# Kernel optimization log

Measured on AMD Instinct MI355X. Metric: run time of the kernel, lower is better.

## Reference

```python
import jax, jax.numpy as jnp
import numpy as np

B, T_IN, T_OUT, N, D_IN, D_OUT, H, L, K = 32, 12, 12, 200, 2, 1, 128, 2, 2
DH = H // 2
M = 2 * K + 1  # identity + K diffusion steps for each of the 2 supports
SQRT_H = float(np.sqrt(H))


def setup_inputs():
    key = jax.random.key(0)
    ks = iter(jax.random.split(key, 40))
    def rn(shape, s=0.1):
        return jax.random.normal(next(ks), shape, dtype=jnp.float32) * s
    return {
        "encoder_inputs": rn((B, T_IN, N, D_IN), 1.0),
        "decoder_inputs": rn((B, T_OUT, N, D_OUT), 1.0),
        "gru_Wih": rn((3 * H, D_IN)), "gru_Whh": rn((3 * H, H)),
        "gru_bih": rn((3 * H,)), "gru_bhh": rn((3 * H,)),
        "att_W": rn((DH, H)), "att_b": rn((DH,)),
        "w_len_C": rn((DH, 1)), "w_key": rn((H, DH)), "w_query": rn((H, DH)),
        "enc_Wg0": rn(((D_IN + H) * M, 2 * H)), "enc_bg0": rn((2 * H,)),
        "enc_Wc0": rn(((D_IN + H) * M, H)), "enc_bc0": rn((H,)),
        "enc_Wg1": rn((2 * H * M, 2 * H)), "enc_bg1": rn((2 * H,)),
        "enc_Wc1": rn((2 * H * M, H)), "enc_bc1": rn((H,)),
        "dec_Wg0": rn(((D_OUT + H) * M, 2 * H)), "dec_bg0": rn((2 * H,)),
        "dec_Wc0": rn(((D_OUT + H) * M, H)), "dec_bc0": rn((H,)),
        "dec_Wg1": rn((2 * H * M, 2 * H)), "dec_bg1": rn((2 * H,)),
        "dec_Wc1": rn((2 * H * M, H)), "dec_bc1": rn((H,)),
        "proj_W": rn((D_OUT, H)), "proj_b": rn((D_OUT,)),
        "top_k": 20,
    }


def _gconv(supports, x, W, b):
    # x: (B, N, D); supports: list of (B, N, N). Chebyshev-style diffusion.
    xs = [x]
    for s in supports:
        x0, x1 = x, jnp.einsum('bij,bjd->bid', s, x)
        xs.append(x1)
        for _ in range(2, K + 1):
            x2 = 2.0 * jnp.einsum('bij,bjd->bid', s, x1) - x0
            xs.append(x2)
            x0, x1 = x1, x2
    xm = jnp.stack(xs, axis=-1).reshape(x.shape[0], x.shape[1], -1)  # (B,N,D*M)
    return xm @ W + b


def _cell(supports, inp, h, Wg, bg, Wc, bc):
    # DCGRU cell: diffusion-conv GRU gating. inp (B,N,di), h (B,N,H)
    ru = jax.nn.sigmoid(_gconv(supports, jnp.concatenate([inp, h], -1), Wg, bg))
    r, u = ru[..., :H], ru[..., H:]
    c = jnp.tanh(_gconv(supports, jnp.concatenate([inp, r * h], -1), Wc, bc))
    return u * h + (1.0 - u) * c


def _supports(x, gru_Wih, gru_Whh, gru_bih, gru_bhh, att_W, att_b, w_len_C, w_key, w_query, top_k):
    # x: (B, T, N, D) -> per-node GRU over time (fold nodes into batch)
    xt = jnp.transpose(x, (1, 2, 0, 3)).reshape(T_IN, N * B, D_IN)
    def gru_step(h, xin):
        gi = xin @ gru_Wih.T + gru_bih
        gh = h @ gru_Whh.T + gru_bhh
        ir, iz, ig = jnp.split(gi, 3, -1)
        hr, hz, hg = jnp.split(gh, 3, -1)
        r = jax.nn.sigmoid(ir + hr)
        z = jax.nn.sigmoid(iz + hz)
        n = jnp.tanh(ig + r * hg)
        hnew = (1.0 - z) * n + z * h
        return hnew, hnew
    _, outs = jax.lax.scan(gru_step, jnp.zeros((N * B, H), x.dtype), xt)
    outs = outs.reshape(T_IN, N, B, H)
    # temporal attention pooling per node
    sc = jax.nn.relu(jnp.einsum('tnbh,dh->tnbd', outs, att_W) + att_b)
    att_t = jax.nn.softmax(jnp.einsum('tnbd,do->tnbo', sc, w_len_C)[..., 0], axis=0)  # (T,N,B)
    pooled = jnp.einsum('tnbh,tnb->bnh', outs, att_t)  # (B,N,H)
    # node-node attention -> sparsified adjacency
    keym = pooled @ w_key
    qm = pooled @ w_query
    attn = jax.nn.softmax(jnp.einsum('bnd,bmd->bnm', keym, qm) / SQRT_H, axis=-1)
    kth = jax.lax.top_k(attn, top_k)[0][..., -1:]  # k-th largest per row
    adj = jnp.where(attn >= kth, attn, 0.0) + jnp.eye(N, dtype=attn.dtype)
    def rw(a):  # D^-1 A, row-normalized random walk
        d = a.sum(-1)
        dinv = jnp.where(d == 0.0, 0.0, 1.0 / d)
        return dinv[..., None] * a
    s1 = jnp.transpose(rw(adj), (0, 2, 1))
    s2 = jnp.transpose(rw(jnp.transpose(adj, (0, 2, 1))), (0, 2, 1))
    return [s1, s2]


def _forward(encoder_inputs, decoder_inputs, gru_Wih, gru_Whh, gru_bih, gru_bhh,
             att_W, att_b, w_len_C, w_key, w_query,
             enc_Wg0, enc_bg0, enc_Wc0, enc_bc0, enc_Wg1, enc_bg1, enc_Wc1, enc_bc1,
             dec_Wg0, dec_bg0, dec_Wc0, dec_bc0, dec_Wg1, dec_bg1, dec_Wc1, dec_bc1,
             proj_W, proj_b, top_k):
    supports = _supports(encoder_inputs, gru_Wih, gru_Whh, gru_bih, gru_bhh,
                         att_W, att_b, w_len_C, w_key, w_query, top_k)
    enc = jnp.transpose(encoder_inputs, (1, 0, 2, 3))  # (T,B,N,Din)
    enc_params = [(enc_Wg0, enc_bg0, enc_Wc0, enc_bc0), (enc_Wg1, enc_bg1, enc_Wc1, enc_bc1)]
    dec_params = [(dec_Wg0, dec_bg0, dec_Wc0, dec_bc0), (dec_Wg1, dec_bg1, dec_Wc1, dec_bc1)]
    # encoder: scan over time per layer
    cur = enc
    hiddens = []
    for l in range(L):
        Wg, bg, Wc, bc = enc_params[l]
        def estep(h, xin, Wg=Wg, bg=bg, Wc=Wc, bc=bc):
            hn = _cell(supports, xin, h, Wg, bg, Wc, bc)
            return hn, hn
        hl, cur = jax.lax.scan(estep, jnp.zeros((B, N, H), enc.dtype), cur)
        hiddens.append(hl)
    go = jnp.zeros((B, N, D_OUT), enc.dtype)
    def dstep(carry, _):
        hs, x = carry
        hs_new = []
        for l in range(L):
            hn = _cell(supports, x, hs[l], *dec_params[l])
            x = hn
            hs_new.append(hn)
        proj = x @ proj_W.T + proj_b  # (B,N,D_OUT)
        return (tuple(hs_new), proj), proj.reshape(B, N * D_OUT)
    _, outputs = jax.lax.scan(dstep, (tuple(hiddens), go), None, length=T_OUT)
    return outputs  # (T_OUT, B, N*D_OUT)


def reference(encoder_inputs, decoder_inputs, gru_Wih, gru_Whh, gru_bih, gru_bhh,
              att_W, att_b, w_len_C, w_key, w_query,
              enc_Wg0, enc_bg0, enc_Wc0, enc_bc0, enc_Wg1, enc_bg1, enc_Wc1, enc_bc1,
              dec_Wg0, dec_bg0, dec_Wc0, dec_bc0, dec_Wg1, dec_bg1, dec_Wc1, dec_bc1,
              proj_W, proj_b, top_k):
    return _forward(encoder_inputs, decoder_inputs, gru_Wih, gru_Whh, gru_bih, gru_bhh,
                    att_W, att_b, w_len_C, w_key, w_query,
                    enc_Wg0, enc_bg0, enc_Wc0, enc_bc0, enc_Wg1, enc_bg1, enc_Wc1, enc_bc1,
                    dec_Wg0, dec_bg0, dec_Wc0, dec_bc0, dec_Wg1, dec_bg1, dec_Wc1, dec_bc1,
                    proj_W, proj_b, top_k)
```

## Files before the change

### kernel.cpp

```cpp
#include <hip/hip_runtime.h>
#include <hip/hip_bf16.h>
#include <math.h>

#define BB 32
#define T_INC 12
#define T_OUTC 12
#define NN 200
#define DIN0 2
#define HH 128
#define DHALF 64
#define NB (NN*BB)
#define XROW 256
#define MSTRIDE ((size_t)NB*XROW)
#define CHUNK 32
#define QT 2
#define KT2 7
#define RT2 13
#define SFRAG_PER_B ((size_t)RT2*KT2*64*8)
#define PANEL_E (KT2*QT*64*8)
#define GCONV_LDS (4*PANEL_E*2)
#define INV_SQRT_H 0.08838834764831845f

typedef __attribute__((ext_vector_type(8))) short bf16x8;
typedef __attribute__((ext_vector_type(4))) float f32x4;

__device__ __forceinline__ float sigmf(float x){ return 1.f/(1.f+expf(-x)); }
__device__ __forceinline__ float bfu(uint32_t b){ union{uint32_t u;float f;}v; v.u=b<<16; return v.f; }
__device__ __forceinline__ uint32_t fbf(float f){ union{float f2;uint32_t u;}v; v.f2=f; return (v.u + 0x7fffu + ((v.u>>16)&1u))>>16; }
__device__ __forceinline__ void splitbf(float v, uint32_t& hi, uint32_t& lo){
  hi = fbf(v);
  lo = fbf(v - bfu(hi));
}

__global__ void k_whhT(const float* __restrict__ Whh, float* __restrict__ WT) {
  int idx = blockIdx.x*256 + threadIdx.x;
  if (idx >= 3*HH*HH) return;
  int i3 = idx / HH; int k = idx % HH;
  WT[(size_t)k*(3*HH) + i3] = Whh[idx];
}

__global__ void k_wshuf(const float* __restrict__ W, __hip_bfloat16* __restrict__ Wfh,
                        __hip_bfloat16* __restrict__ Wfl, int d, int d_pad, int OUT) {
  int idx = blockIdx.x*256 + threadIdx.x;
  int total = 5*d_pad*OUT;
  if (idx >= total) return;
  int o = idx % OUT; int tmp = idx / OUT; int k = tmp % d_pad; int m = tmp / d_pad;
  float v = (k < d) ? W[((size_t)k*5 + m)*OUT + o] : 0.f;
  int kt = k >> 5, kr = k & 31;
  int lane = ((kr>>3)<<4) | (o & 15);
  int j = kr & 7;
  int nt = o >> 4;
  int KT = d_pad >> 5, NT = OUT >> 4;
  size_t addr = ((((size_t)m*KT + kt)*NT + nt)*64 + (size_t)lane)*8 + j;
  uint32_t hi, lo; splitbf(v, hi, lo);
  Wfh[addr] = *(__hip_bfloat16*)&hi;
  Wfl[addr] = *(__hip_bfloat16*)&lo;
}

__global__ void k_sshuf(const float* __restrict__ adj, const float* __restrict__ rs,
                        const float* __restrict__ cs,
                        __hip_bfloat16* __restrict__ SFH, __hip_bfloat16* __restrict__ SFL) {
  const int PER_B = 208*224;
  int idx = blockIdx.x*256 + threadIdx.x;
  if (idx >= 2*BB*PER_B) return;
  int e = idx % PER_B; int t2 = idx / PER_B; int b = t2 % BB; int mat = t2 / BB;
  int n = e / 224; int j = e % 224;
  float v = 0.f;
  if (n < NN && j < NN) {
    if (mat == 0) v = adj[((size_t)b*NN + j)*NN + n] / rs[(size_t)b*NN + j];
    else          v = adj[((size_t)b*NN + n)*NN + j] / cs[(size_t)b*NN + j];
  }
  int rt = n >> 4, rr = n & 15, kt = j >> 5, kr = j & 31;
  int lane = ((kr >> 3) << 4) | rr;
  int jj = kr & 7;
  size_t addr = ((size_t)(mat*BB + b)*RT2*KT2 + (size_t)(rt*KT2 + kt))*512
              + (size_t)lane*8 + jj;
  uint32_t hi, lo; splitbf(v, hi, lo);
  SFH[addr] = *(__hip_bfloat16*)&hi;
  SFL[addr] = *(__hip_bfloat16*)&lo;
}

__global__ __launch_bounds__(512) void k_gru_all(
    const float* __restrict__ enc_in, const float* __restrict__ Wih,
    const float* __restrict__ WhhT, const float* __restrict__ bih,
    const float* __restrict__ bhh, float* __restrict__ outs) {
  int row0 = blockIdx.x * 4;
  int tid = threadIdx.x;
  int rr = tid >> 7;
  int i = tid & 127;
  int row = row0 + rr;
  int n = row / BB, b = row % BB;
  __shared__ float hs[4][HH];
  hs[rr][i] = 0.f;
  float wi0 = Wih[(0*HH+i)*2+0], wi1 = Wih[(0*HH+i)*2+1];
  float wz0 = Wih[(1*HH+i)*2+0], wz1 = Wih[(1*HH+i)*2+1];
  float wg0 = Wih[(2*HH+i)*2+0], wg1 = Wih[(2*HH+i)*2+1];
  float bi = bih[i], bz = bih[HH+i], bg = bih[2*HH+i];
  float bhr = bhh[i], bhz = bhh[HH+i], bhg = bhh[2*HH+i];
  for (int t=0;t<T_INC;t++) {
    __syncthreads();
    float x0 = enc_in[(((size_t)b*T_INC + t)*NN + n)*DIN0 + 0];
    float x1 = enc_in[(((size_t)b*T_INC + t)*NN + n)*DIN0 + 1];
    float ir = wi0*x0 + wi1*x1 + bi;
    float iz = wz0*x0 + wz1*x1 + bz;
    float ig = wg0*x0 + wg1*x1 + bg;
    float hr = bhr, hz = bhz, hg = bhg;
    for (int k=0;k<HH;k++) {
      float hv = hs[rr][k];
      const float* wr = WhhT + (size_t)k*(3*HH);
      hr += wr[i]*hv; hz += wr[i+128]*hv; hg += wr[i+256]*hv;
    }
    float r = sigmf(ir+hr);
    float z = sigmf(iz+hz);
    float nn2 = tanhf(ig + r*hg);
    float hn = (1.f-z)*nn2 + z*hs[rr][i];
    __syncthreads();
    hs[rr][i] = hn;
    outs[(((size_t)t*NN+n)*BB+b)*HH + i] = hn;
  }
}

__global__ __launch_bounds__(256) void k_att_pool(
    const float* __restrict__ outs, const float* __restrict__ attW,
    const float* __restrict__ attb, const float* __restrict__ wlc,
    float* __restrict__ pooled) {
  int row = blockIdx.x; int n = row / BB, b = row % BB;
  int tid = threadIdx.x;
  __shared__ float o_s[T_INC][HH];
  __shared__ float aw[DHALF][HH+1];
  __shared__ float pt[T_INC];
  for (int i = tid; i < T_INC*HH; i += 256) {
    int t = i >> 7, k = i & 127;
    o_s[t][k] = outs[(((size_t)t*NN+n)*BB+b)*HH + k];
  }
  for (int i = tid; i < DHALF*HH; i += 256) {
    int d2 = i >> 7, k = i & 127;
    aw[d2][k] = attW[(size_t)d2*HH + k];
  }
  __syncthreads();
  int d = tid & 63, tq = tid >> 6;
  float ab = attb[d], wc = wlc[d];
  float part[3];
  #pragma unroll
  for (int j=0;j<3;j++) {
    int t = tq + j*4;
    float acc = ab;
    for (int k=0;k<HH;k++) acc += aw[d][k]*o_s[t][k];
    part[j] = fmaxf(acc, 0.f)*wc;
  }
  for (int off=32; off; off>>=1)
    #pragma unroll
    for (int j=0;j<3;j++) part[j] += __shfl_xor(part[j], off, 64);
  if (d == 0) { pt[tq] = part[0]; pt[tq+4] = part[1]; pt[tq+8] = part[2]; }
  __syncthreads();
  float mx = -1e30f;
  for (int t=0;t<T_INC;t++) mx = fmaxf(mx, pt[t]);
  float e[T_INC]; float s = 0.f;
  for (int t=0;t<T_INC;t++) { e[t] = expf(pt[t]-mx); s += e[t]; }
  float inv = 1.f/s;
  for (int k=tid;k<HH;k+=256) {
    float acc = 0.f;
    for (int t=0;t<T_INC;t++) acc += o_s[t][k]*e[t];
    pooled[((size_t)b*NN+n)*HH + k] = acc*inv;
  }
}

__global__ void k_keyquery(const float* __restrict__ pooled, const float* __restrict__ wkey,
                           const float* __restrict__ wqry, float* __restrict__ keym,
                           float* __restrict__ qm) {
  int bn = blockIdx.x; int lane = threadIdx.x;
  __shared__ float p_s[HH];
  p_s[lane] = pooled[(size_t)bn*HH + lane];
  p_s[lane+64] = pooled[(size_t)bn*HH + lane + 64];
  __syncthreads();
  float ka = 0.f, qa = 0.f;
  for (int k=0;k<HH;k++) {
    float pv = p_s[k];
    ka += pv*wkey[(size_t)k*DHALF + lane];
    qa += pv*wqry[(size_t)k*DHALF + lane];
  }
  keym[(size_t)bn*DHALF + lane] = ka;
  qm[(size_t)bn*DHALF + lane] = qa;
}

__global__ void k_attn_row(const float* __restrict__ keym, const float* __restrict__ qm,
                           const int* __restrict__ topkp, float* __restrict__ adj,
                           float* __restrict__ rowsum) {
  int bn = blockIdx.x; int b = bn / NN; int n = bn % NN;
  int tid = threadIdx.x;
  __shared__ float key_s[DHALF];
  __shared__ float attv[256];
  __shared__ float red[256];
  __shared__ int redi[256];
  if (tid < DHALF) key_s[tid] = keym[(size_t)bn*DHALF + tid];
  __syncthreads();
  float sc = -1e30f;
  if (tid < NN) {
    float a = 0.f;
    const float* qrow = qm + ((size_t)b*NN + tid)*DHALF;
    for (int k=0;k<DHALF;k++) a += key_s[k]*qrow[k];
    sc = a * INV_SQRT_H;
  }
  red[tid] = sc; __syncthreads();
  for (int s=128;s>0;s>>=1){ if (tid<s) red[tid]=fmaxf(red[tid],red[tid+s]); __syncthreads(); }
  float mx = red[0]; __syncthreads();
  float e = (tid<NN) ? expf(sc-mx) : 0.f;
  red[tid] = e; __syncthreads();
  for (int s=128;s>0;s>>=1){ if (tid<s) red[tid]+=red[tid+s]; __syncthreads(); }
  float inv = 1.f/red[0]; __syncthreads();
  float av = e*inv;
  attv[tid] = (tid<NN) ? av : -1e30f;
  __syncthreads();
  int Ks = topkp[0]; if (Ks > NN) Ks = NN;
  float kth = -1e30f;
  for (int it=0; it<Ks; it++) {
    red[tid] = attv[tid]; redi[tid] = tid; __syncthreads();
    for (int s=128;s>0;s>>=1){
      if (tid<s && red[tid+s] > red[tid]) { red[tid]=red[tid+s]; redi[tid]=redi[tid+s]; }
      __syncthreads();
    }
    kth = red[0];
    if (tid==0) attv[redi[0]] = -1e30f;
    __syncthreads();
  }
  float aout = 0.f;
  if (tid < NN) {
    aout = (av >= kth) ? av : 0.f;
    if (tid == n) aout += 1.f;
    adj[((size_t)b*NN+n)*NN + tid] = aout;
  }
  red[tid] = aout; __syncthreads();
  for (int s=128;s>0;s>>=1){ if (tid<s) red[tid]+=red[tid+s]; __syncthreads(); }
  if (tid==0) rowsum[bn] = red[0];
}

__global__ void k_colsum(const float* __restrict__ adj, float* __restrict__ cs) {
  int b = blockIdx.x;
  for (int j=threadIdx.x; j<NN; j+=blockDim.x) {
    float s = 0.f;
    for (int i=0;i<NN;i++) s += adj[((size_t)b*NN+i)*NN + j];
    cs[(size_t)b*NN + j] = s;
  }
}

__global__ __launch_bounds__(512) void k_gconv_mfma(
    const float* __restrict__ x, int bs, int ns, int din,
    const float* __restrict__ h, const float* __restrict__ ru,
    const __hip_bfloat16* __restrict__ SFH, const __hip_bfloat16* __restrict__ SFL,
    uint32_t* __restrict__ XP, int d) {
  extern __shared__ char ldsc[];
  ushort* X0H = (ushort*)ldsc;
  ushort* X0L = X0H + PANEL_E;
  ushort* XTH = X0L + PANEL_E;
  ushort* XTL = XTH + PANEL_E;
  int c0 = blockIdx.x*CHUNK;
  int b  = blockIdx.y;
  int tid = threadIdx.x;
  int l = tid & 63, wid = tid >> 6;

  { uint4 z = make_uint4(0,0,0,0);
    uint4* p = (uint4*)ldsc;
    for (int i = tid; i < GCONV_LDS/16; i += 512) p[i] = z; }
  __syncthreads();

  for (int i = tid; i < NN*CHUNK; i += 512) {
    int n = i >> 5, cc = i & 31;
    int c = c0 + cc;
    float v = 0.f;
    if (c < din) {
      v = x[(size_t)b*bs + (size_t)n*ns + c];
    } else if (c < d) {
      int k = c - din;
      v = h[((size_t)(b*NN+n))*HH + k];
      if (ru) v *= ru[(size_t)(b*NN+n)*256 + k];
    }
    uint32_t hi, lo; splitbf(v, hi, lo);
    int kt = n >> 5, kr = n & 31;
    int ln = ((kr>>3)<<4) | (cc & 15), jj = kr & 7, q = cc >> 4;
    int fa = ((kt*QT + q)*64 + ln)*8 + jj;
    X0H[fa] = (ushort)hi; X0L[fa] = (ushort)lo;
    XP[(size_t)(b*NN+n)*XROW + c] = hi | (lo << 16);
  }
  __syncthreads();

  for (int ph = 0; ph < 4; ph++) {
    int side = ph >> 1, cheb = ph & 1;
    const ushort* BH = cheb ? XTH : X0H;
    const ushort* BL = cheb ? XTL : X0L;
    const __hip_bfloat16* AH = SFH + (size_t)(side*BB + b)*SFRAG_PER_B;
    const __hip_bfloat16* AL = SFL + (size_t)(side*BB + b)*SFRAG_PER_B;
    int mout = 1 + ph;
    for (int rt = wid; rt < RT2; rt += 8) {
      f32x4 acc[QT];
      #pragma unroll
      for (int q=0;q<QT;q++) acc[q] = (f32x4){0.f,0.f,0.f,0.f};
      for (int kt = 0; kt < KT2; kt++) {
        size_t aoff = ((size_t)(rt*KT2+kt)*64 + l)*8;
        bf16x8 ah = *(const bf16x8*)(AH + aoff);
        bf16x8 al = *(const bf16x8*)(AL + aoff);
        #pragma unroll
        for (int q=0;q<QT;q++) {
          int boff = ((kt*QT+q)*64 + l)*8;
          bf16x8 bh = *(const bf16x8*)(BH + boff);
          bf16x8 bl = *(const bf16x8*)(BL + boff);
          acc[q] = __builtin_amdgcn_mfma_f32_16x16x32_bf16(ah, bl, acc[q], 0, 0, 0);
          acc[q] = __builtin_amdgcn_mfma_f32_16x16x32_bf16(al, bh, acc[q], 0, 0, 0);
          acc[q] = __builtin_amdgcn_mfma_f32_16x16x32_bf16(ah, bh, acc[q], 0, 0, 0);
        }
      }
      int colb = l & 15;
      #pragma unroll
      for (int q=0;q<QT;q++) {
        int cc = q*16 + colb;
        #pragma unroll
        for (int r=0;r<4;r++) {
          int n = rt*16 + ((l>>4)<<2) + r;
          float v = acc[q][r];
          int kt2 = n >> 5, kr = n & 31;
          int ln = ((kr>>3)<<4) | colb, jj = kr & 7;
          int fa = ((kt2*QT + q)*64 + ln)*8 + jj;
          if (cheb) {
            uint32_t h2 = X0H[fa], l2 = X0L[fa];
            v = 2.f*v - (bfu(h2) + bfu(l2));
          }
          uint32_t hi, lo; splitbf(v, hi, lo);
          if (!cheb) { XTH[fa] = (ushort)hi; XTL[fa] = (ushort)lo; }
          if (n < NN)
            XP[(size_t)mout*MSTRIDE + (size_t)(b*NN+n)*XROW + c0 + cc] = hi | (lo << 16);
        }
      }
    }
    __syncthreads();
  }
}

template<int OUT, int PATH>
__global__ __launch_bounds__(256) void k_dense_mfma(
    const uint32_t* __restrict__ XP,
    const __hip_bfloat16* __restrict__ Wfh, const __hip_bfloat16* __restrict__ Wfl,
    const float* __restrict__ bias, int d_pad,
    float* __restrict__ RU, const float* __restrict__ h, float* __restrict__ hnew,
    const float* __restrict__ pW, const float* __restrict__ pb,
    float* __restrict__ out, float* __restrict__ decx, int t) {
  __shared__ ushort SA[2*32*256];
  ushort* SAh = SA;
  ushort* SAl = SA + 32*256;
  int tid = threadIdx.x;
  int w = tid >> 6, l = tid & 63;
  int rblk = blockIdx.x*32;
  int rbase = (w&1)*16;
  int cbase = blockIdx.y*128 + (w>>1)*64;
  const int NT = OUT >> 4;
  int KT = d_pad >> 5;
  f32x4 acc[4];
  #pragma unroll
  for (int q=0;q<4;q++) acc[q] = (f32x4){0.f,0.f,0.f,0.f};
  size_t boff = (((size_t)(cbase>>4))*64 + l)*8;
  int ngrp = d_pad >> 3;
  for (int m=0;m<5;m++) {
    __syncthreads();
    for (int i = tid; i < 32*ngrp; i += 256) {
      int r = i / ngrp, cg = i % ngrp;
      const uint32_t* gp = XP + (size_t)m*MSTRIDE + (size_t)(rblk+r)*XROW + cg*8;
      uint4 p0 = *(const uint4*)gp;
      uint4 p1 = *(const uint4*)(gp+4);
      uint4 hv, lv;
      hv.x = (p0.x & 0xffffu) | (p0.y << 16);
      hv.y = (p0.z & 0xffffu) | (p0.w << 16);
      hv.z = (p1.x & 0xffffu) | (p1.y << 16);
      hv.w = (p1.z & 0xffffu) | (p1.w << 16);
      lv.x = (p0.x >> 16) | (p0.y & 0xffff0000u);
      lv.y = (p0.z >> 16) | (p0.w & 0xffff0000u);
      lv.z = (p1.x >> 16) | (p1.y & 0xffff0000u);
      lv.w = (p1.z >> 16) | (p1.w & 0xffff0000u);
      uint32_t bo2 = ((uint32_t)(r*256 + cg*8)*2) ^ ((uint32_t)(r&7)<<4);
      *(uint4*)((char*)SAh + bo2) = hv;
      *(uint4*)((char*)SAl + bo2) = lv;
    }
    __syncthreads();
    for (int kt=0; kt<KT; kt++) {
      int rr = rbase + (l & 15);
      uint32_t fb = ((uint32_t)(rr*256 + kt*32 + (l>>4)*8)*2) ^ ((uint32_t)(rr&7)<<4);
      bf16x8 ah = *(const bf16x8*)((const char*)SAh + fb);
      bf16x8 al = *(const bf16x8*)((const char*)SAl + fb);
      size_t bo = boff + ((size_t)(m*KT + kt)*NT)*512;
      #pragma unroll
      for (int q=0;q<4;q++) {
        bf16x8 bh = *(const bf16x8*)(Wfh + bo + (size_t)q*512);
        bf16x8 bl = *(const bf16x8*)(Wfl + bo + (size_t)q*512);
        acc[q] = __builtin_amdgcn_mfma_f32_16x16x32_bf16(ah, bl, acc[q], 0, 0, 0);
        acc[q] = __builtin_amdgcn_mfma_f32_16x16x32_bf16(al, bh, acc[q], 0, 0, 0);
        acc[q] = __builtin_amdgcn_mfma_f32_16x16x32_bf16(ah, bh, acc[q], 0, 0, 0);
      }
    }
  }
  bool doproj = (PATH==1) && (pW != nullptr);
  if (doproj) __syncthreads();
  float* PH = (float*)SA;
  int drow0 = rbase + ((l>>4)<<2);
  int col0 = l & 15;
  #pragma unroll
  for (int q=0;q<4;q++) {
    int col = cbase + q*16 + col0;
    float bv = bias[col];
    #pragma unroll
    for (int r=0;r<4;r++) {
      int rowrel = drow0 + r;
      int row = rblk + rowrel;
      float v = acc[q][r] + bv;
      if (PATH==0) {
        RU[(size_t)row*256 + col] = sigmf(v);
      } else {
        float c = tanhf(v);
        float u = RU[(size_t)row*256 + 128 + col];
        float hv = u*h[(size_t)row*HH + col] + (1.f-u)*c;
        hnew[(size_t)row*HH + col] = hv;
        if (doproj) PH[rowrel*HH + col] = hv;
      }
    }
  }
  if (doproj) {
    __syncthreads();
    int rowrel = tid >> 3;
    int sub = tid & 7;
    float s = 0.f;
    const float* ph = PH + rowrel*HH + sub*16;
    #pragma unroll
    for (int c=0;c<16;c++) s += ph[c]*pW[sub*16 + c];
    s += __shfl_xor(s, 1, 64);
    s += __shfl_xor(s, 2, 64);
    s += __shfl_xor(s, 4, 64);
    if (sub == 0) {
      float pv = s + pb[0];
      int gr = rblk + rowrel;
      out[(size_t)t*NB + gr] = pv;
      decx[gr] = pv;
    }
  }
}

extern "C" void kernel_launch(void* const* d_in, const int* in_sizes, int n_in,
                              void* d_out, int out_size, void* d_ws, size_t ws_size,
                              hipStream_t stream) {
  const float* enc_in = (const float*)d_in[0];
  const float* gWih = (const float*)d_in[2];
  const float* gWhh = (const float*)d_in[3];
  const float* gbih = (const float*)d_in[4];
  const float* gbhh = (const float*)d_in[5];
  const float* attW = (const float*)d_in[6];
  const float* attb = (const float*)d_in[7];
  const float* wlc  = (const float*)d_in[8];
  const float* wkey = (const float*)d_in[9];
  const float* wqry = (const float*)d_in[10];
  const float* cWg[4] = {(const float*)d_in[11],(const float*)d_in[15],(const float*)d_in[19],(const float*)d_in[23]};
  const float* cbg[4] = {(const float*)d_in[12],(const float*)d_in[16],(const float*)d_in[20],(const float*)d_in[24]};
  const float* cWc[4] = {(const float*)d_in[13],(const float*)d_in[17],(const float*)d_in[21],(const float*)d_in[25]};
  const float* cbc[4] = {(const float*)d_in[14],(const float*)d_in[18],(const float*)d_in[22],(const float*)d_in[26]};
  const float* pW = (const float*)d_in[27];
  const float* pb = (const float*)d_in[28];
  const int* topkp = (const int*)d_in[29];
  float* out = (float*)d_out;

  const int d_full[4] = {130, 256, 129, 256};
  const int d_padv[4] = {192, 256, 192, 256};

  float* ws = (float*)d_ws;
  size_t off = 0;
  auto alloc = [&](size_t n) { float* p = ws + off; off += (n + 255) & ~(size_t)255; return p; };

  float* RS   = alloc(NB);
  float* CS   = alloc(NB);
  float* RU   = alloc((size_t)NB*256);
  float* H0A  = alloc((size_t)NB*HH);
  float* H0B  = alloc((size_t)NB*HH);
  float* H1A  = alloc((size_t)NB*HH);
  float* H1B  = alloc((size_t)NB*HH);
  float* DECX = alloc(NB);
  float* WHHT = alloc((size_t)3*HH*HH);
  __hip_bfloat16* SFH = (__hip_bfloat16*)alloc((size_t)2*BB*SFRAG_PER_B/2);
  __hip_bfloat16* SFL = (__hip_bfloat16*)alloc((size_t)2*BB*SFRAG_PER_B/2);
  __hip_bfloat16 *WGFh[4], *WGFl[4], *WCFh[4], *WCFl[4];
  for (int p=0;p<4;p++) {
    WGFh[p] = (__hip_bfloat16*)alloc((size_t)5*d_padv[p]*256/2);
    WGFl[p] = (__hip_bfloat16*)alloc((size_t)5*d_padv[p]*256/2);
    WCFh[p] = (__hip_bfloat16*)alloc((size_t)5*d_padv[p]*128/2);
    WCFl[p] = (__hip_bfloat16*)alloc((size_t)5*d_padv[p]*128/2);
  }

  const size_t SUP_SZ = (size_t)T_INC*NN*BB*HH
                      + (size_t)NB*HH
                      + (size_t)NB*DHALF*2
                      + (size_t)BB*NN*NN + 4096;
  const size_t CELL_SZ = 5*MSTRIDE + 4096;
  float* UNION = alloc(SUP_SZ > CELL_SZ ? SUP_SZ : CELL_SZ);
  float* OUTS = UNION;
  float* POOL = OUTS + (size_t)T_INC*NN*BB*HH;
  float* KEYM = POOL + (size_t)NB*HH;
  float* QMM  = KEYM + (size_t)NB*DHALF;
  float* ADJ  = QMM  + (size_t)NB*DHALF;
  uint32_t* XP = (uint32_t*)UNION;

  if (off*sizeof(float) > ws_size) return;

  hipMemsetAsync(H0A, 0, (size_t)NB*HH*sizeof(float), stream);
  hipMemsetAsync(H1A, 0, (size_t)NB*HH*sizeof(float), stream);
  hipMemsetAsync(DECX, 0, (size_t)NB*sizeof(float), stream);

  k_whhT<<<(3*HH*HH+255)/256, 256, 0, stream>>>(gWhh, WHHT);
  for (int p=0;p<4;p++) {
    int tg = 5*d_padv[p]*256;
    k_wshuf<<<(tg+255)/256, 256, 0, stream>>>(cWg[p], WGFh[p], WGFl[p], d_full[p], d_padv[p], 256);
    int tc = 5*d_padv[p]*128;
    k_wshuf<<<(tc+255)/256, 256, 0, stream>>>(cWc[p], WCFh[p], WCFl[p], d_full[p], d_padv[p], 128);
  }

  k_gru_all<<<NB/4, 512, 0, stream>>>(enc_in, gWih, WHHT, gbih, gbhh, OUTS);
  k_att_pool<<<NB, 256, 0, stream>>>(OUTS, attW, attb, wlc, POOL);
  k_keyquery<<<NB, 64, 0, stream>>>(POOL, wkey, wqry, KEYM, QMM);
  k_attn_row<<<NB, 256, 0, stream>>>(KEYM, QMM, topkp, ADJ, RS);
  k_colsum<<<BB, 256, 0, stream>>>(ADJ, CS);
  { int tot = 2*BB*208*224;
    k_sshuf<<<(tot+255)/256, 256, 0, stream>>>(ADJ, RS, CS, SFH, SFL); }

  auto gconv = [&](const float* x, int bs, int ns, int din, const float* hcur,
                   const float* ru, int pidx) {
    int d = d_full[pidx], dp = d_padv[pidx];
    dim3 gg(dp/CHUNK, BB);
    k_gconv_mfma<<<gg, 512, GCONV_LDS, stream>>>(
        x, bs, ns, din, hcur, ru, SFH, SFL, XP, d);
  };

  auto cell = [&](const float* x, int bs, int ns, int din,
                  float** hcur, float** halt, int pidx, int t) {
    int dp = d_padv[pidx];
    gconv(x, bs, ns, din, *hcur, nullptr, pidx);
    k_dense_mfma<256,0><<<dim3(NB/32,2),256,0,stream>>>(
        XP, WGFh[pidx], WGFl[pidx], cbg[pidx], dp, RU, nullptr, nullptr,
        nullptr, nullptr, nullptr, nullptr, 0);
    gconv(x, bs, ns, din, *hcur, RU, pidx);
    const float* ppW = (pidx == 3) ? pW : nullptr;
    k_dense_mfma<128,1><<<dim3(NB/32,1),256,0,stream>>>(
        XP, WCFh[pidx], WCFl[pidx], cbc[pidx], dp, RU, *hcur, *halt,
        ppW, pb, out, DECX, t);
    float* tswp = *hcur; *hcur = *halt; *halt = tswp;
  };

  float* h0cur = H0A; float* h0alt = H0B;
  float* h1cur = H1A; float* h1alt = H1B;

  for (int t=0;t<T_INC;t++) {
    cell(enc_in + (size_t)t*NN*DIN0, T_INC*NN*DIN0, DIN0, DIN0, &h0cur, &h0alt, 0, 0);
    cell(h0cur, NN*HH, HH, HH, &h1cur, &h1alt, 1, 0);
  }
  for (int t=0;t<T_OUTC;t++) {
    cell(DECX, NN, 1, 1, &h0cur, &h0alt, 2, t);
    cell(h0cur, NN*HH, HH, HH, &h1cur, &h1alt, 3, t);
  }
}
```

Before: 9.072 ms.

## Restructure gconv phases, double-buffer dense loads, widen GRU rows per block

The GRU kernel now handles 16 rows per block with 4 rows per thread, so each Whh weight load is reused across rows. The diffusion gconv kernel merges the two supports into a single task loop and keeps separate LDS panels for each side, cutting the four barrier-separated phases down to two at the cost of more LDS. The dense MFMA kernel prefetches the next slab into registers and double-buffers it in LDS. The candidate path uses 16-row blocks so more blocks run, and the projection reduction is adjusted to match. The extra LDS and registers may lower occupancy.

```diff
diff --git a/kernel.cpp b/kernel.cpp
--- a/kernel.cpp
+++ b/kernel.cpp
@@ -18,7 +18,8 @@
 #define RT2 13
 #define SFRAG_PER_B ((size_t)RT2*KT2*64*8)
 #define PANEL_E (KT2*QT*64*8)
-#define GCONV_LDS (4*PANEL_E*2)
+#define GCONV_LDS6 (6*PANEL_E*2)
+#define GRU_ROWS 16
 #define INV_SQRT_H 0.08838834764831845f
 
 typedef __attribute__((ext_vector_type(8))) short bf16x8;
@@ -84,39 +85,56 @@
     const float* __restrict__ enc_in, const float* __restrict__ Wih,
     const float* __restrict__ WhhT, const float* __restrict__ bih,
     const float* __restrict__ bhh, float* __restrict__ outs) {
-  int row0 = blockIdx.x * 4;
+  int row0 = blockIdx.x * GRU_ROWS;
   int tid = threadIdx.x;
-  int rr = tid >> 7;
+  int g = tid >> 7;
   int i = tid & 127;
-  int row = row0 + rr;
-  int n = row / BB, b = row % BB;
-  __shared__ float hs[4][HH];
-  hs[rr][i] = 0.f;
+  __shared__ float hs[GRU_ROWS][HH];
+  #pragma unroll
+  for (int j=0;j<4;j++) hs[g+4*j][i] = 0.f;
   float wi0 = Wih[(0*HH+i)*2+0], wi1 = Wih[(0*HH+i)*2+1];
   float wz0 = Wih[(1*HH+i)*2+0], wz1 = Wih[(1*HH+i)*2+1];
   float wg0 = Wih[(2*HH+i)*2+0], wg1 = Wih[(2*HH+i)*2+1];
   float bi = bih[i], bz = bih[HH+i], bg = bih[2*HH+i];
   float bhr = bhh[i], bhz = bhh[HH+i], bhg = bhh[2*HH+i];
+  int nn_[4], bb_[4];
+  #pragma unroll
+  for (int j=0;j<4;j++) { int r = row0 + g + 4*j; nn_[j] = r / BB; bb_[j] = r % BB; }
   for (int t=0;t<T_INC;t++) {
     __syncthreads();
-    float x0 = enc_in[(((size_t)b*T_INC + t)*NN + n)*DIN0 + 0];
-    float x1 = enc_in[(((size_t)b*T_INC + t)*NN + n)*DIN0 + 1];
-    float ir = wi0*x0 + wi1*x1 + bi;
-    float iz = wz0*x0 + wz1*x1 + bz;
-    float ig = wg0*x0 + wg1*x1 + bg;
-    float hr = bhr, hz = bhz, hg = bhg;
+    float hr[4], hz[4], hg[4], ii_[4], iz_[4], ig_[4];
+    #pragma unroll
+    for (int j=0;j<4;j++) {
+      float x0 = enc_in[(((size_t)bb_[j]*T_INC + t)*NN + nn_[j])*DIN0 + 0];
+      float x1 = enc_in[(((size_t)bb_[j]*T_INC + t)*NN + nn_[j])*DIN0 + 1];
+      ii_[j] = wi0*x0 + wi1*x1 + bi;
+      iz_[j] = wz0*x0 + wz1*x1 + bz;
+      ig_[j] = wg0*x0 + wg1*x1 + bg;
+      hr[j] = bhr; hz[j] = bhz; hg[j] = bhg;
+    }
     for (int k=0;k<HH;k++) {
-      float hv = hs[rr][k];
       const float* wr = WhhT + (size_t)k*(3*HH);
-      hr += wr[i]*hv; hz += wr[i+128]*hv; hg += wr[i+256]*hv;
-    }
-    float r = sigmf(ir+hr);
-    float z = sigmf(iz+hz);
-    float nn2 = tanhf(ig + r*hg);
-    float hn = (1.f-z)*nn2 + z*hs[rr][i];
+      float w0 = wr[i], w1 = wr[i+128], w2 = wr[i+256];
+      #pragma unroll
+      for (int j=0;j<4;j++) {
+        float hv = hs[g+4*j][k];
+        hr[j] += w0*hv; hz[j] += w1*hv; hg[j] += w2*hv;
+      }
+    }
+    float hn[4];
+    #pragma unroll
+    for (int j=0;j<4;j++) {
+      float r = sigmf(ii_[j]+hr[j]);
+      float z = sigmf(iz_[j]+hz[j]);
+      float nn2 = tanhf(ig_[j] + r*hg[j]);
+      hn[j] = (1.f-z)*nn2 + z*hs[g+4*j][i];
+    }
     __syncthreads();
-    hs[rr][i] = hn;
-    outs[(((size_t)t*NN+n)*BB+b)*HH + i] = hn;
+    #pragma unroll
+    for (int j=0;j<4;j++) {
+      hs[g+4*j][i] = hn[j];
+      outs[(((size_t)t*NN+nn_[j])*BB+bb_[j])*HH + i] = hn[j];
+    }
   }
 }
 
@@ -251,8 +269,10 @@
   extern __shared__ char ldsc[];
   ushort* X0H = (ushort*)ldsc;
   ushort* X0L = X0H + PANEL_E;
-  ushort* XTH = X0L + PANEL_E;
-  ushort* XTL = XTH + PANEL_E;
+  ushort* T1H = X0L + PANEL_E;
+  ushort* T1L = T1H + PANEL_E;
+  ushort* T2H = T1L + PANEL_E;
+  ushort* T2L = T2H + PANEL_E;
   int c0 = blockIdx.x*CHUNK;
   int b  = blockIdx.y;
   int tid = threadIdx.x;
@@ -260,7 +280,7 @@
 
   { uint4 z = make_uint4(0,0,0,0);
     uint4* p = (uint4*)ldsc;
-    for (int i = tid; i < GCONV_LDS/16; i += 512) p[i] = z; }
+    for (int i = tid; i < GCONV_LDS6/16; i += 512) p[i] = z; }
   __syncthreads();
 
   for (int i = tid; i < NN*CHUNK; i += 512) {
@@ -283,54 +303,92 @@
   }
   __syncthreads();
 
-  for (int ph = 0; ph < 4; ph++) {
-    int side = ph >> 1, cheb = ph & 1;
-    const ushort* BH = cheb ? XTH : X0H;
-    const ushort* BL = cheb ? XTL : X0L;
+  for (int task = wid; task < 2*RT2; task += 8) {
+    int side = task & 1, rt = task >> 1;
     const __hip_bfloat16* AH = SFH + (size_t)(side*BB + b)*SFRAG_PER_B;
     const __hip_bfloat16* AL = SFL + (size_t)(side*BB + b)*SFRAG_PER_B;
-    int mout = 1 + ph;
-    for (int rt = wid; rt < RT2; rt += 8) {
-      f32x4 acc[QT];
-      #pragma unroll
-      for (int q=0;q<QT;q++) acc[q] = (f32x4){0.f,0.f,0.f,0.f};
-      for (int kt = 0; kt < KT2; kt++) {
-        size_t aoff = ((size_t)(rt*KT2+kt)*64 + l)*8;
-        bf16x8 ah = *(const bf16x8*)(AH + aoff);
-        bf16x8 al = *(const bf16x8*)(AL + aoff);
-        #pragma unroll
-        for (int q=0;q<QT;q++) {
-          int boff = ((kt*QT+q)*64 + l)*8;
-          bf16x8 bh = *(const bf16x8*)(BH + boff);
-          bf16x8 bl = *(const bf16x8*)(BL + boff);
-          acc[q] = __builtin_amdgcn_mfma_f32_16x16x32_bf16(ah, bl, acc[q], 0, 0, 0);
-          acc[q] = __builtin_amdgcn_mfma_f32_16x16x32_bf16(al, bh, acc[q], 0, 0, 0);
-          acc[q] = __builtin_amdgcn_mfma_f32_16x16x32_bf16(ah, bh, acc[q], 0, 0, 0);
-        }
-      }
-      int colb = l & 15;
+    ushort* TH = side ? T2H : T1H;
+    ushort* TL = side ? T2L : T1L;
+    int mout = 1 + 2*side;
+    f32x4 acc[QT];
+    #pragma unroll
+    for (int q=0;q<QT;q++) acc[q] = (f32x4){0.f,0.f,0.f,0.f};
+    for (int kt = 0; kt < KT2; kt++) {
+      size_t aoff = ((size_t)(rt*KT2+kt)*64 + l)*8;
+      bf16x8 ah = *(const bf16x8*)(AH + aoff);
+      bf16x8 al = *(const bf16x8*)(AL + aoff);
       #pragma unroll
       for (int q=0;q<QT;q++) {
-        int cc = q*16 + colb;
-        #pragma unroll
-        for (int r=0;r<4;r++) {
-          int n = rt*16 + ((l>>4)<<2) + r;
-          float v = acc[q][r];
-          int kt2 = n >> 5, kr = n & 31;
-          int ln = ((kr>>3)<<4) | colb, jj = kr & 7;
-          int fa = ((kt2*QT + q)*64 + ln)*8 + jj;
-          if (cheb) {
-            uint32_t h2 = X0H[fa], l2 = X0L[fa];
-            v = 2.f*v - (bfu(h2) + bfu(l2));
-          }
-          uint32_t hi, lo; splitbf(v, hi, lo);
-          if (!cheb) { XTH[fa] = (ushort)hi; XTL[fa] = (ushort)lo; }
-          if (n < NN)
-            XP[(size_t)mout*MSTRIDE + (size_t)(b*NN+n)*XROW + c0 + cc] = hi | (lo << 16);
-        }
+        int boff = ((kt*QT+q)*64 + l)*8;
+        bf16x8 bh = *(const bf16x8*)(X0H + boff);
+        bf16x8 bl = *(const bf16x8*)(X0L + boff);
+        acc[q] = __builtin_amdgcn_mfma_f32_16x16x32_bf16(ah, bl, acc[q], 0, 0, 0);
+        acc[q] = __builtin_amdgcn_mfma_f32_16x16x32_bf16(al, bh, acc[q], 0, 0, 0);
+        acc[q] = __builtin_amdgcn_mfma_f32_16x16x32_bf16(ah, bh, acc[q], 0, 0, 0);
       }
     }
-    __syncthreads();
+    int colb = l & 15;
+    #pragma unroll
+    for (int q=0;q<QT;q++) {
+      int cc = q*16 + colb;
+      #pragma unroll
+      for (int r=0;r<4;r++) {
+        int n = rt*16 + ((l>>4)<<2) + r;
+        float v = acc[q][r];
+        int kt2 = n >> 5, kr = n & 31;
+        int ln = ((kr>>3)<<4) | colb, jj = kr & 7;
+        int fa = ((kt2*QT + q)*64 + ln)*8 + jj;
+        uint32_t hi, lo; splitbf(v, hi, lo);
+        TH[fa] = (ushort)hi; TL[fa] = (ushort)lo;
+        if (n < NN)
+          XP[(size_t)mout*MSTRIDE + (size_t)(b*NN+n)*XROW + c0 + cc] = hi | (lo << 16);
+      }
+    }
+  }
+  __syncthreads();
+
+  for (int task = wid; task < 2*RT2; task += 8) {
+    int side = task & 1, rt = task >> 1;
+    const __hip_bfloat16* AH = SFH + (size_t)(side*BB + b)*SFRAG_PER_B;
+    const __hip_bfloat16* AL = SFL + (size_t)(side*BB + b)*SFRAG_PER_B;
+    const ushort* BH = side ? T2H : T1H;
+    const ushort* BL = side ? T2L : T1L;
+    int mout = 2 + 2*side;
+    f32x4 acc[QT];
+    #pragma unroll
+    for (int q=0;q<QT;q++) acc[q] = (f32x4){0.f,0.f,0.f,0.f};
+    for (int kt = 0; kt < KT2; kt++) {
+      size_t aoff = ((size_t)(rt*KT2+kt)*64 + l)*8;
+      bf16x8 ah = *(const bf16x8*)(AH + aoff);
+      bf16x8 al = *(const bf16x8*)(AL + aoff);
+      #pragma unroll
+      for (int q=0;q<QT;q++) {
+        int boff = ((kt*QT+q)*64 + l)*8;
+        bf16x8 bh = *(const bf16x8*)(BH + boff);
+        bf16x8 bl = *(const bf16x8*)(BL + boff);
+        acc[q] = __builtin_amdgcn_mfma_f32_16x16x32_bf16(ah, bl, acc[q], 0, 0, 0);
+        acc[q] = __builtin_amdgcn_mfma_f32_16x16x32_bf16(al, bh, acc[q], 0, 0, 0);
+        acc[q] = __builtin_amdgcn_mfma_f32_16x16x32_bf16(ah, bh, acc[q], 0, 0, 0);
+      }
+    }
+    int colb = l & 15;
+    #pragma unroll
+    for (int q=0;q<QT;q++) {
+      int cc = q*16 + colb;
+      #pragma unroll
+      for (int r=0;r<4;r++) {
+        int n = rt*16 + ((l>>4)<<2) + r;
+        float v = acc[q][r];
+        int kt2 = n >> 5, kr = n & 31;
+        int ln = ((kr>>3)<<4) | colb, jj = kr & 7;
+        int fa = ((kt2*QT + q)*64 + ln)*8 + jj;
+        uint32_t h2 = X0H[fa], l2 = X0L[fa];
+        v = 2.f*v - (bfu(h2) + bfu(l2));
+        uint32_t hi, lo; splitbf(v, hi, lo);
+        if (n < NN)
+          XP[(size_t)mout*MSTRIDE + (size_t)(b*NN+n)*XROW + c0 + cc] = hi | (lo << 16);
+      }
+    }
   }
 }
 
@@ -342,28 +400,41 @@
     float* __restrict__ RU, const float* __restrict__ h, float* __restrict__ hnew,
     const float* __restrict__ pW, const float* __restrict__ pb,
     float* __restrict__ out, float* __restrict__ decx, int t) {
-  __shared__ ushort SA[2*32*256];
-  ushort* SAh = SA;
-  ushort* SAl = SA + 32*256;
+  constexpr int ROWS  = (PATH==0) ? 32 : 16;
+  constexpr int NQ    = (PATH==0) ? 4  : 2;
+  constexpr int MAXIT = (PATH==0) ? 4  : 2;
+  __shared__ ushort SA[2][2*ROWS*256];
   int tid = threadIdx.x;
   int w = tid >> 6, l = tid & 63;
-  int rblk = blockIdx.x*32;
-  int rbase = (w&1)*16;
-  int cbase = blockIdx.y*128 + (w>>1)*64;
+  int rblk = blockIdx.x*ROWS;
+  int rbase = (PATH==0) ? (w&1)*16 : 0;
+  int cbase = (PATH==0) ? ((int)blockIdx.y*128 + (w>>1)*64) : (w*NQ*16);
   const int NT = OUT >> 4;
   int KT = d_pad >> 5;
-  f32x4 acc[4];
+  f32x4 acc[NQ];
   #pragma unroll
-  for (int q=0;q<4;q++) acc[q] = (f32x4){0.f,0.f,0.f,0.f};
+  for (int q=0;q<NQ;q++) acc[q] = (f32x4){0.f,0.f,0.f,0.f};
   size_t boff = (((size_t)(cbase>>4))*64 + l)*8;
   int ngrp = d_pad >> 3;
-  for (int m=0;m<5;m++) {
-    __syncthreads();
-    for (int i = tid; i < 32*ngrp; i += 256) {
-      int r = i / ngrp, cg = i % ngrp;
+  int total = ROWS*ngrp;
+  uint4 pf0[MAXIT], pf1[MAXIT];
+
+  auto issue = [&](int m){
+    int c2 = 0;
+    for (int i2 = tid; i2 < total; i2 += 256, c2++) {
+      int r = i2 / ngrp, cg = i2 % ngrp;
       const uint32_t* gp = XP + (size_t)m*MSTRIDE + (size_t)(rblk+r)*XROW + cg*8;
-      uint4 p0 = *(const uint4*)gp;
-      uint4 p1 = *(const uint4*)(gp+4);
+      pf0[c2] = *(const uint4*)gp;
+      pf1[c2] = *(const uint4*)(gp+4);
+    }
+  };
+  auto commit = [&](int buf){
+    ushort* SAh = SA[buf];
+    ushort* SAl = SA[buf] + ROWS*256;
+    int c2 = 0;
+    for (int i2 = tid; i2 < total; i2 += 256, c2++) {
+      int r = i2 / ngrp, cg = i2 % ngrp;
+      uint4 p0 = pf0[c2], p1 = pf1[c2];
       uint4 hv, lv;
       hv.x = (p0.x & 0xffffu) | (p0.y << 16);
       hv.y = (p0.z & 0xffffu) | (p0.w << 16);
@@ -377,7 +448,14 @@
       *(uint4*)((char*)SAh + bo2) = hv;
       *(uint4*)((char*)SAl + bo2) = lv;
     }
+  };
+
+  issue(0); commit(0);
+  for (int m=0;m<5;m++) {
+    if (m < 4) issue(m+1);
     __syncthreads();
+    const ushort* SAh = SA[m&1];
+    const ushort* SAl = SA[m&1] + ROWS*256;
     for (int kt=0; kt<KT; kt++) {
       int rr = rbase + (l & 15);
       uint32_t fb = ((uint32_t)(rr*256 + kt*32 + (l>>4)*8)*2) ^ ((uint32_t)(rr&7)<<4);
@@ -385,7 +463,7 @@
       bf16x8 al = *(const bf16x8*)((const char*)SAl + fb);
       size_t bo = boff + ((size_t)(m*KT + kt)*NT)*512;
       #pragma unroll
-      for (int q=0;q<4;q++) {
+      for (int q=0;q<NQ;q++) {
         bf16x8 bh = *(const bf16x8*)(Wfh + bo + (size_t)q*512);
         bf16x8 bl = *(const bf16x8*)(Wfl + bo + (size_t)q*512);
         acc[q] = __builtin_amdgcn_mfma_f32_16x16x32_bf16(ah, bl, acc[q], 0, 0, 0);
@@ -393,6 +471,7 @@
         acc[q] = __builtin_amdgcn_mfma_f32_16x16x32_bf16(ah, bh, acc[q], 0, 0, 0);
       }
     }
+    if (m < 4) commit((m+1)&1);
   }
   bool doproj = (PATH==1) && (pW != nullptr);
   if (doproj) __syncthreads();
@@ -400,7 +479,7 @@
   int drow0 = rbase + ((l>>4)<<2);
   int col0 = l & 15;
   #pragma unroll
-  for (int q=0;q<4;q++) {
+  for (int q=0;q<NQ;q++) {
     int col = cbase + q*16 + col0;
     float bv = bias[col];
     #pragma unroll
@@ -421,15 +500,16 @@
   }
   if (doproj) {
     __syncthreads();
-    int rowrel = tid >> 3;
-    int sub = tid & 7;
+    int rowrel = tid >> 4;
+    int sub = tid & 15;
     float s = 0.f;
-    const float* ph = PH + rowrel*HH + sub*16;
-    #pragma unroll
-    for (int c=0;c<16;c++) s += ph[c]*pW[sub*16 + c];
+    const float* ph = PH + rowrel*HH + sub*8;
+    #pragma unroll
+    for (int c=0;c<8;c++) s += ph[c]*pW[sub*8 + c];
     s += __shfl_xor(s, 1, 64);
     s += __shfl_xor(s, 2, 64);
     s += __shfl_xor(s, 4, 64);
+    s += __shfl_xor(s, 8, 64);
     if (sub == 0) {
       float pv = s + pb[0];
       int gr = rblk + rowrel;
@@ -514,7 +594,7 @@
     k_wshuf<<<(tc+255)/256, 256, 0, stream>>>(cWc[p], WCFh[p], WCFl[p], d_full[p], d_padv[p], 128);
   }
 
-  k_gru_all<<<NB/4, 512, 0, stream>>>(enc_in, gWih, WHHT, gbih, gbhh, OUTS);
+  k_gru_all<<<NB/GRU_ROWS, 512, 0, stream>>>(enc_in, gWih, WHHT, gbih, gbhh, OUTS);
   k_att_pool<<<NB, 256, 0, stream>>>(OUTS, attW, attb, wlc, POOL);
   k_keyquery<<<NB, 64, 0, stream>>>(POOL, wkey, wqry, KEYM, QMM);
   k_attn_row<<<NB, 256, 0, stream>>>(KEYM, QMM, topkp, ADJ, RS);
@@ -526,7 +606,7 @@
                    const float* ru, int pidx) {
     int d = d_full[pidx], dp = d_padv[pidx];
     dim3 gg(dp/CHUNK, BB);
-    k_gconv_mfma<<<gg, 512, GCONV_LDS, stream>>>(
+    k_gconv_mfma<<<gg, 512, GCONV_LDS6, stream>>>(
         x, bs, ns, din, hcur, ru, SFH, SFL, XP, d);
   };
 
@@ -539,7 +619,7 @@
         nullptr, nullptr, nullptr, nullptr, 0);
     gconv(x, bs, ns, din, *hcur, RU, pidx);
     const float* ppW = (pidx == 3) ? pW : nullptr;
-    k_dense_mfma<128,1><<<dim3(NB/32,1),256,0,stream>>>(
+    k_dense_mfma<128,1><<<dim3(NB/16,1),256,0,stream>>>(
         XP, WCFh[pidx], WCFl[pidx], cbc[pidx], dp, RU, *hcur, *halt,
         ppW, pb, out, DECX, t);
     float* tswp = *hcur; *hcur = *halt; *halt = tswp;
```

New measurement: 9.123 ms. Within noise of the previous version (+0.6%).
